# Performance work log

Measured on AMD Instinct MI355X. Metric: run time of the kernel, lower is better.

Reference implementation:

```python
import jax, jax.numpy as jnp
import numpy as np

N = 150000   # total supergraph nodes (entities+events+chains)
D = 128      # embed_size
H = 4        # attention heads
DH = D // H  # head dim
E = 300000   # edges per layer
L = 4        # layer_specs length
A = 8        # edge attr dim
T = 10       # num_edge_type
TIME_SCALE = 24.0
SLOPE = 0.2  # negative_slope


def setup_inputs() -> dict:
    key = jax.random.key(0)
    ks = jax.random.split(key, 16)
    nrm = lambda k, s, sc=1.0: jax.random.normal(k, s, dtype=jnp.float32) * sc
    return {
        'x': nrm(ks[0], (N, D), 0.1),
        'Wq': nrm(ks[1], (L, D, D), D ** -0.5),
        'Wk': nrm(ks[2], (L, D, D), D ** -0.5),
        'Wv': nrm(ks[3], (L, D, D), D ** -0.5),
        'Wskip': nrm(ks[4], (L, D, D), D ** -0.5),
        'Wa': nrm(ks[5], (L, A, D), 0.1),
        'time_w': nrm(ks[6], (D,)),
        'time_b': nrm(ks[7], (D,), 0.1),
        'dist_w': nrm(ks[8], (D,)),
        'dist_b': nrm(ks[9], (D,), 0.1),
        'type_table': nrm(ks[10], (T, D), 0.1),
        'bn_gamma': jnp.ones((L, D), jnp.float32),
        'bn_beta': jnp.zeros((L, D), jnp.float32),
        'beta': jnp.full((L,), 0.5, jnp.float32),
        'edge_attr': jax.random.uniform(ks[11], (L, E, A), dtype=jnp.float32),
        'edge_dt': jax.random.uniform(ks[12], (L, E), dtype=jnp.float32) * TIME_SCALE,
        'edge_ds': jax.random.uniform(ks[13], (L, E), dtype=jnp.float32) * 10.0,
        'edge_index': jax.random.randint(ks[14], (L, 2, E), 0, N),
        'edge_type': jax.random.randint(ks[15], (L, E), 0, T),
    }


def _layer(x, Wq, Wk, Wv, Wskip, Wa, time_w, time_b, dist_w, dist_b,
           type_table, gamma, bvec, beta, attr, dt, ds, ei, et):
    n = x.shape[0]
    src, dst = ei[0], ei[1]
    # continuous time / distance encoders: cos basis (TimeEncoder / 'time' DistanceEncoder)
    te = jnp.cos((dt / TIME_SCALE)[:, None] * time_w + time_b)   # [E,D]
    de = jnp.cos(ds[:, None] * dist_w + dist_b)                  # [E,D]
    # 'add' edge/time fusion: attr MLP + time + dist + edge-type embeddings
    edge_feat = attr @ Wa + te + de + type_table[et]             # [E,D]
    kv_in = x[src] + edge_feat                                   # gather + fuse
    q = (x @ Wq).reshape(n, H, DH)[dst]                          # [E,H,DH]
    k = (kv_in @ Wk).reshape(-1, H, DH)
    v = (kv_in @ Wv).reshape(-1, H, DH)
    logits = (q * k).sum(-1) * (DH ** -0.5)                      # [E,H]
    logits = jnp.where(logits >= 0, logits, SLOPE * logits)      # leaky_relu(negative_slope)
    # segment softmax over incoming edges of each destination node
    m = jax.ops.segment_max(logits, dst, num_segments=n)
    a = jnp.exp(logits - m[dst])
    denom = jax.ops.segment_sum(a, dst, num_segments=n)
    a = a / denom[dst]
    agg = jax.ops.segment_sum(a[..., None] * v, dst, num_segments=n).reshape(n, D)
    # beta-weighted residual (learn_beta) with skip projection
    out = beta * (x @ Wskip) + (1.0 - beta) * agg
    # BatchNorm1d (training-mode batch stats) + ReLU
    mu = out.mean(0)
    var = out.var(0)
    out = (out - mu) * jax.lax.rsqrt(var + 1e-5) * gamma + bvec
    return jax.nn.relu(out)


def reference(x, Wq, Wk, Wv, Wskip, Wa, time_w, time_b, dist_w, dist_b,
              type_table, bn_gamma, bn_beta, beta, edge_attr, edge_dt,
              edge_ds, edge_index, edge_type):
    for l in range(L):  # entity2event, event2event, event2chain (time filter), chain2chain
        x = _layer(x, Wq[l], Wk[l], Wv[l], Wskip[l], Wa[l],
                   time_w, time_b, dist_w, dist_b, type_table,
                   bn_gamma[l], bn_beta[l], beta[l],
                   edge_attr[l], edge_dt[l], edge_ds[l],
                   edge_index[l], edge_type[l])
    return x
```

## Files before the change

kernel.cpp:

```cpp
#include <hip/hip_runtime.h>

typedef unsigned int u32;
typedef unsigned short u16;
typedef short bf16x8 __attribute__((ext_vector_type(8)));
typedef float f32x4 __attribute__((ext_vector_type(4)));

#define N_NODES 150000
#define E_EDGES 300000
#define L_CNT   151552

__device__ __forceinline__ float b2f(u16 h){ return __uint_as_float(((u32)h) << 16); }
__device__ __forceinline__ u16 f2bf(float f){
  u32 u = __float_as_uint(f);
  return (u16)((u + 0x7fffu + ((u >> 16) & 1u)) >> 16);
}

__device__ __forceinline__ f32x4 mfma16(bf16x8 a, bf16x8 b, f32x4 c){
  return __builtin_amdgcn_mfma_f32_16x16x32_bf16(a, b, c, 0, 0, 0);
}

__device__ __forceinline__ int opsw(int r, int k){ return (r * 128 + k) ^ ((r & 7) << 3); }
__device__ __forceinline__ int csw(int r, int n){ return (r * 128 + n) ^ (((r >> 2) & 3) << 3); }

__global__ __launch_bounds__(256)
void k_wt(const float* __restrict__ Wq, const float* __restrict__ Wk,
          const float* __restrict__ Wv, const float* __restrict__ Ws,
          u16* __restrict__ Wt)
{
  const int m = blockIdx.x;
  const float* src = (m < 4 ? Wq : m < 8 ? Wk : m < 12 ? Wv : Ws)
                     + (size_t)(m & 3) * 16384;
  u16* dst = Wt + (size_t)m * 16384;
  const int t = threadIdx.x;
  for (int i = 0; i < 16; ++i) {
    int idx = i * 256 + t;
    int n = idx >> 5;
    int k4 = (idx & 31) << 2;
    ushort4 o;
    o.x = f2bf(src[(k4 + 0) * 128 + n]);
    o.y = f2bf(src[(k4 + 1) * 128 + n]);
    o.z = f2bf(src[(k4 + 2) * 128 + n]);
    o.w = f2bf(src[(k4 + 3) * 128 + n]);
    *(ushort4*)(dst + n * 128 + k4) = o;
  }
}


__device__ __forceinline__ void acc_zero(f32x4 (&acc)[2][8])
{
  #pragma unroll
  for (int a = 0; a < 2; ++a)
    #pragma unroll
    for (int b = 0; b < 8; ++b) {
      acc[a][b][0] = 0.f; acc[a][b][1] = 0.f;
      acc[a][b][2] = 0.f; acc[a][b][3] = 0.f;
    }
}

__device__ __forceinline__ void acc_to_lds(u16* Cs, f32x4 (&acc)[2][8], int lane)
{
  const int lr = lane & 15;
  const int g4 = (lane >> 4) << 2;
  #pragma unroll
  for (int mt = 0; mt < 2; ++mt)
    #pragma unroll
    for (int nt = 0; nt < 8; ++nt)
      #pragma unroll
      for (int j = 0; j < 4; ++j)
        Cs[csw(mt * 16 + g4 + j, nt * 16 + lr)] = f2bf(acc[mt][nt][j]);
}

__device__ __forceinline__ void lds_to_global(const u16* Cs, u16* __restrict__ G,
                                              int base, int nr, int lane)
{
  #pragma unroll
  for (int i = 0; i < 8; ++i) {
    int idx = i * 64 + lane;
    int r = idx >> 4, n8 = (idx & 15) << 3;
    if (r < nr) {
      uint4 v = *(const uint4*)(Cs + csw(r, n8));
      *(uint4*)(G + (size_t)(base + r) * 128 + n8) = v;
    }
  }
}


__global__ __launch_bounds__(256)
void k_hist(const int* __restrict__ eidx, int* __restrict__ counts)
{
  const int l = blockIdx.y;
  const int e = blockIdx.x * 256 + threadIdx.x;
  if (e < E_EDGES) {
    int dst = eidx[(size_t)l * 2 * E_EDGES + E_EDGES + e];
    atomicAdd(&counts[(size_t)l * L_CNT + dst], 1);
  }
}

__global__ __launch_bounds__(256)
void k_scan1(const int* __restrict__ counts, int* __restrict__ rowptr,
             int* __restrict__ bsum)
{
  __shared__ int sh[256];
  const int b = blockIdx.x, l = blockIdx.y;
  const int t = threadIdx.x;
  const int* c = counts + (size_t)l * L_CNT + b * 2048;
  int* rp = rowptr + (size_t)l * L_CNT + b * 2048;
  int v[8]; int s = 0;
  #pragma unroll
  for (int j = 0; j < 8; ++j) { v[j] = c[t * 8 + j]; s += v[j]; }
  sh[t] = s; __syncthreads();
  for (int off = 1; off < 256; off <<= 1) {
    int x = (t >= off) ? sh[t - off] : 0;
    __syncthreads();
    sh[t] += x;
    __syncthreads();
  }
  int excl = (t == 0) ? 0 : sh[t - 1];
  if (t == 255) bsum[l * 128 + b] = sh[255];
  int run = excl;
  #pragma unroll
  for (int j = 0; j < 8; ++j) { rp[t * 8 + j] = run; run += v[j]; }
}

__global__ __launch_bounds__(128)
void k_scan2(int* __restrict__ bsum)
{
  __shared__ int sh[128];
  const int l = blockIdx.x, t = threadIdx.x;
  int v = (t < 74) ? bsum[l * 128 + t] : 0;
  sh[t] = v; __syncthreads();
  for (int off = 1; off < 128; off <<= 1) {
    int x = (t >= off) ? sh[t - off] : 0;
    __syncthreads();
    sh[t] += x;
    __syncthreads();
  }
  int excl = (t == 0) ? 0 : sh[t - 1];
  if (t < 74) bsum[l * 128 + t] = excl;
}

__global__ __launch_bounds__(256)
void k_scan3(int* __restrict__ rowptr, int* __restrict__ tmp,
             const int* __restrict__ bsum)
{
  const int l = blockIdx.y;
  const int q = blockIdx.x * 256 + threadIdx.x;
  int v = rowptr[(size_t)l * L_CNT + q] + bsum[l * 128 + (q >> 11)];
  rowptr[(size_t)l * L_CNT + q] = v;
  tmp[(size_t)l * L_CNT + q] = v;
}

__global__ __launch_bounds__(256)
void k_scatter(const int* __restrict__ eidx, int* __restrict__ tmp,
               int* __restrict__ sorted)
{
  const int l = blockIdx.y;
  const int e = blockIdx.x * 256 + threadIdx.x;
  if (e < E_EDGES) {
    int dst = eidx[(size_t)l * 2 * E_EDGES + E_EDGES + e];
    int pos = atomicAdd(&tmp[(size_t)l * L_CNT + dst], 1);
    sorted[(size_t)l * E_EDGES + pos] = e;
  }
}


template<int XF32>
__global__ __launch_bounds__(256)
void gemm_qs(const void* __restrict__ xg, const u16* __restrict__ WtQ,
             const u16* __restrict__ WtS, u16* __restrict__ Qo,
             u16* __restrict__ So)
{
  __shared__ __align__(16) u16 AsAll[4][4160];
  const int t = threadIdx.x;
  const int w = t >> 6, lane = t & 63;
  u16* As = AsAll[w];
  const int lr = lane & 15, hi = lane >> 4;
  const int tile = blockIdx.x * 4 + w;
  const int row0 = tile * 32;
  if (row0 >= N_NODES) return;
  const int nr = min(32, N_NODES - row0);
  const int g = lane >> 5;
  const int c4 = (lane & 31) << 2;

  #pragma unroll
  for (int i = 0; i < 16; ++i) {
    int r = i * 2 + g;
    ushort4 o = make_ushort4(0, 0, 0, 0);
    if (r < nr) {
      if (XF32) {
        float4 v = *(const float4*)((const float*)xg + (size_t)(row0 + r) * 128 + c4);
        o.x = f2bf(v.x); o.y = f2bf(v.y); o.z = f2bf(v.z); o.w = f2bf(v.w);
      } else {
        o = *(const ushort4*)((const u16*)xg + (size_t)(row0 + r) * 128 + c4);
      }
    }
    *(ushort4*)(As + opsw(r, c4)) = o;
  }

  f32x4 qacc[2][8], sacc[2][8];
  acc_zero(qacc); acc_zero(sacc);
  #pragma unroll
  for (int ks = 0; ks < 4; ++ks) {
    const int kb = ks * 32 + hi * 8;
    bf16x8 a0 = *(const bf16x8*)(As + opsw(lr, kb));
    bf16x8 a1 = *(const bf16x8*)(As + opsw(16 + lr, kb));
    #pragma unroll
    for (int nb = 0; nb < 8; ++nb) {
      bf16x8 bq = *(const bf16x8*)(WtQ + (nb * 16 + lr) * 128 + kb);
      bf16x8 bs = *(const bf16x8*)(WtS + (nb * 16 + lr) * 128 + kb);
      qacc[0][nb] = mfma16(a0, bq, qacc[0][nb]);
      qacc[1][nb] = mfma16(a1, bq, qacc[1][nb]);
      sacc[0][nb] = mfma16(a0, bs, sacc[0][nb]);
      sacc[1][nb] = mfma16(a1, bs, sacc[1][nb]);
    }
  }
  acc_to_lds(As, qacc, lane);
  lds_to_global(As, Qo, row0, nr, lane);
  acc_to_lds(As, sacc, lane);
  lds_to_global(As, So, row0, nr, lane);
}


template<int XF32>
__global__ __launch_bounds__(256)
void edge_pass(const void* __restrict__ xg, const u16* __restrict__ WtK,
               const u16* __restrict__ WtV, const float* __restrict__ Wa,
               const float* __restrict__ tw, const float* __restrict__ tb,
               const float* __restrict__ dw, const float* __restrict__ db,
               const float* __restrict__ ttab, const float* __restrict__ attr,
               const float* __restrict__ dt, const float* __restrict__ dsv,
               const int* __restrict__ srcA, const int* __restrict__ dstA,
               const int* __restrict__ etA, const int* __restrict__ sortedE,
               const u16* __restrict__ Qb, float* __restrict__ logits,
               u16* __restrict__ Vs)
{
  __shared__ __align__(16) u16 AsAll[4][4160];
  __shared__ int dstShAll[4][32];
  const int t = threadIdx.x;
  const int w = t >> 6, lane = t & 63;
  u16* As = AsAll[w];
  int* dstSh = dstShAll[w];
  const int lr = lane & 15, hi = lane >> 4;
  const int tile = blockIdx.x * 4 + w;
  const int e0 = tile * 32;
  if (e0 >= E_EDGES) return;
  const int ne = min(32, E_EDGES - e0);
  const int g = lane >> 5;
  const int c4 = (lane & 31) << 2;

  float4 tw4 = *(const float4*)(tw + c4);
  float4 tb4 = *(const float4*)(tb + c4);
  float4 dw4 = *(const float4*)(dw + c4);
  float4 db4 = *(const float4*)(db + c4);
  float4 wa4[8];
  #pragma unroll
  for (int a = 0; a < 8; ++a) wa4[a] = *(const float4*)(Wa + a * 128 + c4);

  #pragma unroll
  for (int i = 0; i < 16; ++i) {
    int r = i * 2 + g;
    ushort4 o = make_ushort4(0, 0, 0, 0);
    if (r < ne) {
      int eid = sortedE[e0 + r];
      if ((lane & 31) == 0) dstSh[r] = dstA[eid];
      int et = etA[eid];
      float dtn = dt[eid] * (1.0f / 24.0f);
      float dss = dsv[eid];
      float4 tt4 = *(const float4*)(ttab + et * 128 + c4);
      float f0 = __cosf(fmaf(dtn, tw4.x, tb4.x)) + __cosf(fmaf(dss, dw4.x, db4.x)) + tt4.x;
      float f1 = __cosf(fmaf(dtn, tw4.y, tb4.y)) + __cosf(fmaf(dss, dw4.y, db4.y)) + tt4.y;
      float f2 = __cosf(fmaf(dtn, tw4.z, tb4.z)) + __cosf(fmaf(dss, dw4.z, db4.z)) + tt4.z;
      float f3 = __cosf(fmaf(dtn, tw4.w, tb4.w)) + __cosf(fmaf(dss, dw4.w, db4.w)) + tt4.w;
      const float* ap = attr + (size_t)eid * 8;
      #pragma unroll
      for (int a = 0; a < 8; ++a) {
        float aa = ap[a];
        f0 = fmaf(aa, wa4[a].x, f0);
        f1 = fmaf(aa, wa4[a].y, f1);
        f2 = fmaf(aa, wa4[a].z, f2);
        f3 = fmaf(aa, wa4[a].w, f3);
      }
      int src = srcA[eid];
      float x0, x1, x2, x3;
      if (XF32) {
        float4 xr = *(const float4*)((const float*)xg + (size_t)src * 128 + c4);
        x0 = xr.x; x1 = xr.y; x2 = xr.z; x3 = xr.w;
      } else {
        ushort4 xr = *(const ushort4*)((const u16*)xg + (size_t)src * 128 + c4);
        x0 = b2f(xr.x); x1 = b2f(xr.y); x2 = b2f(xr.z); x3 = b2f(xr.w);
      }
      o.x = f2bf(x0 + f0);
      o.y = f2bf(x1 + f1);
      o.z = f2bf(x2 + f2);
      o.w = f2bf(x3 + f3);
    } else {
      if ((lane & 31) == 0) dstSh[r] = 0;
    }
    *(ushort4*)(As + opsw(r, c4)) = o;
  }

  f32x4 kacc[2][8];
  acc_zero(kacc);
  #pragma unroll
  for (int ks = 0; ks < 4; ++ks) {
    const int kb = ks * 32 + hi * 8;
    bf16x8 ef0 = *(const bf16x8*)(As + opsw(lr, kb));
    bf16x8 ef1 = *(const bf16x8*)(As + opsw(16 + lr, kb));
    #pragma unroll
    for (int nb = 0; nb < 8; ++nb) {
      bf16x8 af = *(const bf16x8*)(WtK + (nb * 16 + lr) * 128 + kb);
      kacc[0][nb] = mfma16(af, ef0, kacc[0][nb]);
      kacc[1][nb] = mfma16(af, ef1, kacc[1][nb]);
    }
  }

  #pragma unroll
  for (int eb = 0; eb < 2; ++eb) {
    int el = eb * 16 + lr;
    int dstn = dstSh[el];
    float hs[4] = {0.f, 0.f, 0.f, 0.f};
    #pragma unroll
    for (int nb = 0; nb < 8; ++nb) {
      ushort4 q = *(const ushort4*)(Qb + (size_t)dstn * 128 + nb * 16 + hi * 4);
      hs[nb >> 1] += b2f(q.x) * kacc[eb][nb][0] + b2f(q.y) * kacc[eb][nb][1]
                   + b2f(q.z) * kacc[eb][nb][2] + b2f(q.w) * kacc[eb][nb][3];
    }
    #pragma unroll
    for (int h = 0; h < 4; ++h) {
      hs[h] += __shfl_xor(hs[h], 16, 64);
      hs[h] += __shfl_xor(hs[h], 32, 64);
      hs[h] *= 0.17677669529663687f;
      hs[h] = (hs[h] >= 0.f) ? hs[h] : 0.2f * hs[h];
    }
    if (lane < 16 && el < ne)
      *(float4*)(logits + (size_t)(e0 + el) * 4) = make_float4(hs[0], hs[1], hs[2], hs[3]);
  }

  f32x4 vacc[2][8];
  acc_zero(vacc);
  #pragma unroll
  for (int ks = 0; ks < 4; ++ks) {
    const int kb = ks * 32 + hi * 8;
    bf16x8 af0 = *(const bf16x8*)(As + opsw(lr, kb));
    bf16x8 af1 = *(const bf16x8*)(As + opsw(16 + lr, kb));
    #pragma unroll
    for (int nb = 0; nb < 8; ++nb) {
      bf16x8 bf = *(const bf16x8*)(WtV + (nb * 16 + lr) * 128 + kb);
      vacc[0][nb] = mfma16(af0, bf, vacc[0][nb]);
      vacc[1][nb] = mfma16(af1, bf, vacc[1][nb]);
    }
  }
  acc_to_lds(As, vacc, lane);
  lds_to_global(As, Vs, e0, ne, lane);
}

__global__ __launch_bounds__(256)
void node_agg(const u16* __restrict__ Vs, const float* __restrict__ logits,
              const int* __restrict__ rowptr, const u16* __restrict__ S,
              const float* __restrict__ betaP, float* __restrict__ pre,
              float* __restrict__ colsum, float* __restrict__ colsumsq)
{
  __shared__ float red[1024];
  const int t = threadIdx.x;
  const int g = t >> 5;
  const int lane = t & 31;
  const int d0 = lane * 4;
  const int h = lane >> 3;
  const float beta = *betaP;
  const float omb = 1.f - beta;
  float s4[4] = {0.f, 0.f, 0.f, 0.f};
  float q4[4] = {0.f, 0.f, 0.f, 0.f};
  for (int rep = 0; rep < 16; ++rep) {
    int n = blockIdx.x * 128 + rep * 8 + g;
    if (n < N_NODES) {
      int rs = rowptr[n], re = rowptr[n + 1];
      float m = -1e30f;
      for (int i = rs; i < re; ++i)
        m = fmaxf(m, logits[(size_t)i * 4 + h]);
      float den = 0.f;
      float a0 = 0.f, a1 = 0.f, a2 = 0.f, a3 = 0.f;
      for (int i = rs; i < re; ++i) {
        float wgt = __expf(logits[(size_t)i * 4 + h] - m);
        den += wgt;
        ushort4 v = *(const ushort4*)(Vs + (size_t)i * 128 + d0);
        a0 = fmaf(wgt, b2f(v.x), a0);
        a1 = fmaf(wgt, b2f(v.y), a1);
        a2 = fmaf(wgt, b2f(v.z), a2);
        a3 = fmaf(wgt, b2f(v.w), a3);
      }
      float inv = (den > 0.f) ? (omb / den) : 0.f;
      ushort4 sv = *(const ushort4*)(S + (size_t)n * 128 + d0);
      float p0 = fmaf(beta, b2f(sv.x), a0 * inv);
      float p1 = fmaf(beta, b2f(sv.y), a1 * inv);
      float p2 = fmaf(beta, b2f(sv.z), a2 * inv);
      float p3 = fmaf(beta, b2f(sv.w), a3 * inv);
      *(float4*)(pre + (size_t)n * 128 + d0) = make_float4(p0, p1, p2, p3);
      s4[0] += p0; s4[1] += p1; s4[2] += p2; s4[3] += p3;
      q4[0] += p0 * p0; q4[1] += p1 * p1; q4[2] += p2 * p2; q4[3] += p3 * p3;
    }
  }
  *(float4*)(&red[g * 128 + d0]) = make_float4(s4[0], s4[1], s4[2], s4[3]);
  __syncthreads();
  if (t < 128) {
    float tot = 0.f;
    #pragma unroll
    for (int gg = 0; gg < 8; ++gg) tot += red[gg * 128 + t];
    atomicAdd(&colsum[t], tot);
  }
  __syncthreads();
  *(float4*)(&red[g * 128 + d0]) = make_float4(q4[0], q4[1], q4[2], q4[3]);
  __syncthreads();
  if (t < 128) {
    float tot = 0.f;
    #pragma unroll
    for (int gg = 0; gg < 8; ++gg) tot += red[gg * 128 + t];
    atomicAdd(&colsumsq[t], tot);
  }
}

template<int LAST>
__global__ __launch_bounds__(256)
void bn_apply(const float* __restrict__ pre, const float* __restrict__ colsum,
              const float* __restrict__ colsumsq, const float* __restrict__ gamma,
              const float* __restrict__ bvec, u16* __restrict__ outbf,
              float* __restrict__ outf)
{
  const int idx = blockIdx.x * 256 + threadIdx.x;
  const int n = idx >> 5;
  const int d0 = (idx & 31) * 4;
  const float invN = 1.f / 150000.f;
  float4 p = *(const float4*)(pre + (size_t)n * 128 + d0);
  float4 cs = *(const float4*)(colsum + d0);
  float4 cq = *(const float4*)(colsumsq + d0);
  float4 gm = *(const float4*)(gamma + d0);
  float4 bv = *(const float4*)(bvec + d0);
  float mu, var, y;
  mu = cs.x * invN; var = cq.x * invN - mu * mu;
  y = (p.x - mu) * rsqrtf(var + 1e-5f) * gm.x + bv.x; p.x = fmaxf(y, 0.f);
  mu = cs.y * invN; var = cq.y * invN - mu * mu;
  y = (p.y - mu) * rsqrtf(var + 1e-5f) * gm.y + bv.y; p.y = fmaxf(y, 0.f);
  mu = cs.z * invN; var = cq.z * invN - mu * mu;
  y = (p.z - mu) * rsqrtf(var + 1e-5f) * gm.z + bv.z; p.z = fmaxf(y, 0.f);
  mu = cs.w * invN; var = cq.w * invN - mu * mu;
  y = (p.w - mu) * rsqrtf(var + 1e-5f) * gm.w + bv.w; p.w = fmaxf(y, 0.f);
  if (LAST) {
    *(float4*)(outf + (size_t)n * 128 + d0) = p;
  } else {
    ushort4 o;
    o.x = f2bf(p.x); o.y = f2bf(p.y); o.z = f2bf(p.z); o.w = f2bf(p.w);
    *(ushort4*)(outbf + (size_t)n * 128 + d0) = o;
  }
}

extern "C" void kernel_launch(void* const* d_in, const int* in_sizes, int n_in,
                              void* d_out, int out_size, void* d_ws, size_t ws_size,
                              hipStream_t stream)
{
  const float* x0    = (const float*)d_in[0];
  const float* Wq    = (const float*)d_in[1];
  const float* Wk    = (const float*)d_in[2];
  const float* Wv    = (const float*)d_in[3];
  const float* Wsk   = (const float*)d_in[4];
  const float* Wa    = (const float*)d_in[5];
  const float* tw    = (const float*)d_in[6];
  const float* tb    = (const float*)d_in[7];
  const float* dw    = (const float*)d_in[8];
  const float* db    = (const float*)d_in[9];
  const float* ttab  = (const float*)d_in[10];
  const float* gam   = (const float*)d_in[11];
  const float* bet   = (const float*)d_in[12];
  const float* betaP = (const float*)d_in[13];
  const float* attr  = (const float*)d_in[14];
  const float* dt    = (const float*)d_in[15];
  const float* dsv   = (const float*)d_in[16];
  const int*   eidx  = (const int*)d_in[17];
  const int*   etyp  = (const int*)d_in[18];

  char* p = (char*)d_ws;
  u16* xbf  = (u16*)p;       p += 38400000;
  u16* Q    = (u16*)p;       p += 38400000;
  u16* S    = (u16*)p;       p += 38400000;
  u16* Vs   = (u16*)p;       p += 76800000;
  float* logits = (float*)p; p += 4800000;
  int* rowptr = (int*)p;     p += 4 * L_CNT * 4;
  int* tmp    = (int*)p;     p += 4 * L_CNT * 4;
  int* sorted = (int*)p;     p += 4 * E_EDGES * 4;
  int* bsum   = (int*)p;     p += 4 * 128 * 4;
  float* colsum   = (float*)p; p += 512;
  float* colsumsq = (float*)p; p += 512;
  u16* Wt = (u16*)p;         p += 16 * 16384 * 2;

  float* pre = (float*)d_out;

  k_wt<<<16, 256, 0, stream>>>(Wq, Wk, Wv, Wsk, Wt);
  hipMemsetAsync(tmp, 0, 4 * L_CNT * 4, stream);
  k_hist<<<dim3(1172, 4), 256, 0, stream>>>(eidx, tmp);
  k_scan1<<<dim3(74, 4), 256, 0, stream>>>(tmp, rowptr, bsum);
  k_scan2<<<4, 128, 0, stream>>>(bsum);
  k_scan3<<<dim3(592, 4), 256, 0, stream>>>(rowptr, tmp, bsum);
  k_scatter<<<dim3(1172, 4), 256, 0, stream>>>(eidx, tmp, sorted);

  for (int l = 0; l < 4; ++l) {
    const int* srcA = eidx + (size_t)l * 600000;
    const int* dstA = srcA + 300000;
    const int* sortedE = sorted + (size_t)l * E_EDGES;
    const int* rpl = rowptr + (size_t)l * L_CNT;
    const u16* WtQl = Wt + (size_t)l * 16384;
    const u16* WtKl = Wt + (size_t)(4 + l) * 16384;
    const u16* WtVl = Wt + (size_t)(8 + l) * 16384;
    const u16* WtSl = Wt + (size_t)(12 + l) * 16384;
    const float* Wal = Wa + (size_t)l * 1024;
    const float* attrl = attr + (size_t)l * 2400000;
    const float* dtl = dt + (size_t)l * 300000;
    const float* dsl = dsv + (size_t)l * 300000;
    const int* etl = etyp + (size_t)l * 300000;

    hipMemsetAsync(colsum, 0, 1024, stream);

    if (l == 0) {
      gemm_qs<1><<<1172, 256, 0, stream>>>((const void*)x0, WtQl, WtSl, Q, S);
      edge_pass<1><<<2344, 256, 0, stream>>>(
          (const void*)x0, WtKl, WtVl, Wal, tw, tb, dw, db, ttab, attrl,
          dtl, dsl, srcA, dstA, etl, sortedE, Q, logits, Vs);
    } else {
      gemm_qs<0><<<1172, 256, 0, stream>>>((const void*)xbf, WtQl, WtSl, Q, S);
      edge_pass<0><<<2344, 256, 0, stream>>>(
          (const void*)xbf, WtKl, WtVl, Wal, tw, tb, dw, db, ttab, attrl,
          dtl, dsl, srcA, dstA, etl, sortedE, Q, logits, Vs);
    }

    node_agg<<<1172, 256, 0, stream>>>(Vs, logits, rpl, S, betaP + l,
                                       pre, colsum, colsumsq);

    if (l < 3)
      bn_apply<0><<<18750, 256, 0, stream>>>(pre, colsum, colsumsq,
                                             gam + (size_t)l * 128,
                                             bet + (size_t)l * 128, xbf, nullptr);
    else
      bn_apply<1><<<18750, 256, 0, stream>>>(pre, colsum, colsumsq,
                                             gam + (size_t)l * 128,
                                             bet + (size_t)l * 128,
                                             nullptr, (float*)d_out);
  }
}
```

Baseline: 1.707 ms.

## Pack sorted per-edge metadata in scatter, shrink blocks and split Q/skip GEMM

The scatter kernel now runs once per layer and writes a packed 32-byte record per edge into destination-sorted order: src, dst with edge type, scaled dt, ds, and bf16-packed attributes. The edge pass then reads these records contiguously instead of making indirect gathers through a sorted index. The Q and skip GEMMs are split across a second grid dimension, blocks shrink to 128 threads with a min-blocks launch bound, and the K/V accumulators are computed in halves to lower register pressure and raise occupancy. The risks are precision loss from bf16 edge attributes and four extra scatter launches.

```diff
diff --git a/kernel.cpp b/kernel.cpp
--- a/kernel.cpp
+++ b/kernel.cpp
@@ -9,10 +9,15 @@
 #define E_EDGES 300000
 #define L_CNT   151552
 
+__device__ __forceinline__ float blo(u32 u){ return __uint_as_float(u << 16); }
+__device__ __forceinline__ float bhi(u32 u){ return __uint_as_float(u & 0xffff0000u); }
 __device__ __forceinline__ float b2f(u16 h){ return __uint_as_float(((u32)h) << 16); }
 __device__ __forceinline__ u16 f2bf(float f){
   u32 u = __float_as_uint(f);
   return (u16)((u + 0x7fffu + ((u >> 16) & 1u)) >> 16);
+}
+__device__ __forceinline__ u32 pack2(float a, float b){
+  return (u32)f2bf(a) | ((u32)f2bf(b) << 16);
 }
 
 __device__ __forceinline__ f32x4 mfma16(bf16x8 a, bf16x8 b, f32x4 c){
@@ -45,31 +50,6 @@
   }
 }
 
-
-__device__ __forceinline__ void acc_zero(f32x4 (&acc)[2][8])
-{
-  #pragma unroll
-  for (int a = 0; a < 2; ++a)
-    #pragma unroll
-    for (int b = 0; b < 8; ++b) {
-      acc[a][b][0] = 0.f; acc[a][b][1] = 0.f;
-      acc[a][b][2] = 0.f; acc[a][b][3] = 0.f;
-    }
-}
-
-__device__ __forceinline__ void acc_to_lds(u16* Cs, f32x4 (&acc)[2][8], int lane)
-{
-  const int lr = lane & 15;
-  const int g4 = (lane >> 4) << 2;
-  #pragma unroll
-  for (int mt = 0; mt < 2; ++mt)
-    #pragma unroll
-    for (int nt = 0; nt < 8; ++nt)
-      #pragma unroll
-      for (int j = 0; j < 4; ++j)
-        Cs[csw(mt * 16 + g4 + j, nt * 16 + lr)] = f2bf(acc[mt][nt][j]);
-}
-
 __device__ __forceinline__ void lds_to_global(const u16* Cs, u16* __restrict__ G,
                                               int base, int nr, int lane)
 {
@@ -151,31 +131,49 @@
 }
 
 __global__ __launch_bounds__(256)
-void k_scatter(const int* __restrict__ eidx, int* __restrict__ tmp,
-               int* __restrict__ sorted)
-{
-  const int l = blockIdx.y;
+void k_scatter(const int* __restrict__ srcP, const int* __restrict__ dstP,
+               const int* __restrict__ etP, const float* __restrict__ dtP,
+               const float* __restrict__ dsP, const float* __restrict__ attrP,
+               int* __restrict__ tmpL, u32* __restrict__ meta)
+{
   const int e = blockIdx.x * 256 + threadIdx.x;
   if (e < E_EDGES) {
-    int dst = eidx[(size_t)l * 2 * E_EDGES + E_EDGES + e];
-    int pos = atomicAdd(&tmp[(size_t)l * L_CNT + dst], 1);
-    sorted[(size_t)l * E_EDGES + pos] = e;
+    int dst = dstP[e];
+    int pos = atomicAdd(&tmpL[dst], 1);
+    int src = srcP[e];
+    int et  = etP[e];
+    float dtn = dtP[e] * (1.0f / 24.0f);
+    float dsv = dsP[e];
+    float4 aA = *(const float4*)(attrP + (size_t)e * 8);
+    float4 aB = *(const float4*)(attrP + (size_t)e * 8 + 4);
+    uint4 r0, r1;
+    r0.x = (u32)src;
+    r0.y = (u32)dst | ((u32)et << 20);
+    r0.z = __float_as_uint(dtn);
+    r0.w = __float_as_uint(dsv);
+    r1.x = pack2(aA.x, aA.y); r1.y = pack2(aA.z, aA.w);
+    r1.z = pack2(aB.x, aB.y); r1.w = pack2(aB.z, aB.w);
+    u32* mp = meta + (size_t)pos * 8;
+    *(uint4*)mp = r0;
+    *(uint4*)(mp + 4) = r1;
   }
 }
 
 
 template<int XF32>
-__global__ __launch_bounds__(256)
+__global__ __launch_bounds__(128, 5)
 void gemm_qs(const void* __restrict__ xg, const u16* __restrict__ WtQ,
              const u16* __restrict__ WtS, u16* __restrict__ Qo,
              u16* __restrict__ So)
 {
-  __shared__ __align__(16) u16 AsAll[4][4160];
+  __shared__ __align__(16) u16 AsAll[2][4160];
+  const u16* Wt = blockIdx.y ? WtS : WtQ;
+  u16* C = blockIdx.y ? So : Qo;
   const int t = threadIdx.x;
   const int w = t >> 6, lane = t & 63;
   u16* As = AsAll[w];
   const int lr = lane & 15, hi = lane >> 4;
-  const int tile = blockIdx.x * 4 + w;
+  const int tile = blockIdx.x * 2 + w;
   const int row0 = tile * 32;
   if (row0 >= N_NODES) return;
   const int nr = min(32, N_NODES - row0);
@@ -197,8 +195,14 @@
     *(ushort4*)(As + opsw(r, c4)) = o;
   }
 
-  f32x4 qacc[2][8], sacc[2][8];
-  acc_zero(qacc); acc_zero(sacc);
+  f32x4 acc[2][8];
+  #pragma unroll
+  for (int a = 0; a < 2; ++a)
+    #pragma unroll
+    for (int b = 0; b < 8; ++b) {
+      acc[a][b][0] = 0.f; acc[a][b][1] = 0.f;
+      acc[a][b][2] = 0.f; acc[a][b][3] = 0.f;
+    }
   #pragma unroll
   for (int ks = 0; ks < 4; ++ks) {
     const int kb = ks * 32 + hi * 8;
@@ -206,42 +210,41 @@
     bf16x8 a1 = *(const bf16x8*)(As + opsw(16 + lr, kb));
     #pragma unroll
     for (int nb = 0; nb < 8; ++nb) {
-      bf16x8 bq = *(const bf16x8*)(WtQ + (nb * 16 + lr) * 128 + kb);
-      bf16x8 bs = *(const bf16x8*)(WtS + (nb * 16 + lr) * 128 + kb);
-      qacc[0][nb] = mfma16(a0, bq, qacc[0][nb]);
-      qacc[1][nb] = mfma16(a1, bq, qacc[1][nb]);
-      sacc[0][nb] = mfma16(a0, bs, sacc[0][nb]);
-      sacc[1][nb] = mfma16(a1, bs, sacc[1][nb]);
-    }
-  }
-  acc_to_lds(As, qacc, lane);
-  lds_to_global(As, Qo, row0, nr, lane);
-  acc_to_lds(As, sacc, lane);
-  lds_to_global(As, So, row0, nr, lane);
+      bf16x8 b = *(const bf16x8*)(Wt + (nb * 16 + lr) * 128 + kb);
+      acc[0][nb] = mfma16(a0, b, acc[0][nb]);
+      acc[1][nb] = mfma16(a1, b, acc[1][nb]);
+    }
+  }
+  const int g4 = hi << 2;
+  #pragma unroll
+  for (int mt = 0; mt < 2; ++mt)
+    #pragma unroll
+    for (int nt = 0; nt < 8; ++nt)
+      #pragma unroll
+      for (int j = 0; j < 4; ++j)
+        As[csw(mt * 16 + g4 + j, nt * 16 + lr)] = f2bf(acc[mt][nt][j]);
+  lds_to_global(As, C, row0, nr, lane);
 }
 
 
 template<int XF32>
-__global__ __launch_bounds__(256)
+__global__ __launch_bounds__(128, 5)
 void edge_pass(const void* __restrict__ xg, const u16* __restrict__ WtK,
                const u16* __restrict__ WtV, const float* __restrict__ Wa,
                const float* __restrict__ tw, const float* __restrict__ tb,
                const float* __restrict__ dw, const float* __restrict__ db,
-               const float* __restrict__ ttab, const float* __restrict__ attr,
-               const float* __restrict__ dt, const float* __restrict__ dsv,
-               const int* __restrict__ srcA, const int* __restrict__ dstA,
-               const int* __restrict__ etA, const int* __restrict__ sortedE,
+               const float* __restrict__ ttab, const u32* __restrict__ meta,
                const u16* __restrict__ Qb, float* __restrict__ logits,
                u16* __restrict__ Vs)
 {
-  __shared__ __align__(16) u16 AsAll[4][4160];
-  __shared__ int dstShAll[4][32];
+  __shared__ __align__(16) u16 AsAll[2][4160];
+  __shared__ int dstShAll[2][32];
   const int t = threadIdx.x;
   const int w = t >> 6, lane = t & 63;
   u16* As = AsAll[w];
   int* dstSh = dstShAll[w];
   const int lr = lane & 15, hi = lane >> 4;
-  const int tile = blockIdx.x * 4 + w;
+  const int tile = blockIdx.x * 2 + w;
   const int e0 = tile * 32;
   if (e0 >= E_EDGES) return;
   const int ne = min(32, E_EDGES - e0);
@@ -261,26 +264,28 @@
     int r = i * 2 + g;
     ushort4 o = make_ushort4(0, 0, 0, 0);
     if (r < ne) {
-      int eid = sortedE[e0 + r];
-      if ((lane & 31) == 0) dstSh[r] = dstA[eid];
-      int et = etA[eid];
-      float dtn = dt[eid] * (1.0f / 24.0f);
-      float dss = dsv[eid];
+      const u32* mp = meta + (size_t)(e0 + r) * 8;
+      uint4 m0 = *(const uint4*)mp;
+      uint4 m1 = *(const uint4*)(mp + 4);
+      int src = (int)m0.x;
+      if ((lane & 31) == 0) dstSh[r] = (int)(m0.y & 0xFFFFFu);
+      int et = (int)(m0.y >> 20);
+      float dtn = __uint_as_float(m0.z);
+      float dss = __uint_as_float(m0.w);
       float4 tt4 = *(const float4*)(ttab + et * 128 + c4);
       float f0 = __cosf(fmaf(dtn, tw4.x, tb4.x)) + __cosf(fmaf(dss, dw4.x, db4.x)) + tt4.x;
       float f1 = __cosf(fmaf(dtn, tw4.y, tb4.y)) + __cosf(fmaf(dss, dw4.y, db4.y)) + tt4.y;
       float f2 = __cosf(fmaf(dtn, tw4.z, tb4.z)) + __cosf(fmaf(dss, dw4.z, db4.z)) + tt4.z;
       float f3 = __cosf(fmaf(dtn, tw4.w, tb4.w)) + __cosf(fmaf(dss, dw4.w, db4.w)) + tt4.w;
-      const float* ap = attr + (size_t)eid * 8;
+      float aa[8] = { blo(m1.x), bhi(m1.x), blo(m1.y), bhi(m1.y),
+                      blo(m1.z), bhi(m1.z), blo(m1.w), bhi(m1.w) };
       #pragma unroll
       for (int a = 0; a < 8; ++a) {
-        float aa = ap[a];
-        f0 = fmaf(aa, wa4[a].x, f0);
-        f1 = fmaf(aa, wa4[a].y, f1);
-        f2 = fmaf(aa, wa4[a].z, f2);
-        f3 = fmaf(aa, wa4[a].w, f3);
+        f0 = fmaf(aa[a], wa4[a].x, f0);
+        f1 = fmaf(aa[a], wa4[a].y, f1);
+        f2 = fmaf(aa[a], wa4[a].z, f2);
+        f3 = fmaf(aa[a], wa4[a].w, f3);
       }
-      int src = srcA[eid];
       float x0, x1, x2, x3;
       if (XF32) {
         float4 xr = *(const float4*)((const float*)xg + (size_t)src * 128 + c4);
@@ -299,31 +304,31 @@
     *(ushort4*)(As + opsw(r, c4)) = o;
   }
 
-  f32x4 kacc[2][8];
-  acc_zero(kacc);
-  #pragma unroll
-  for (int ks = 0; ks < 4; ++ks) {
-    const int kb = ks * 32 + hi * 8;
-    bf16x8 ef0 = *(const bf16x8*)(As + opsw(lr, kb));
-    bf16x8 ef1 = *(const bf16x8*)(As + opsw(16 + lr, kb));
-    #pragma unroll
-    for (int nb = 0; nb < 8; ++nb) {
-      bf16x8 af = *(const bf16x8*)(WtK + (nb * 16 + lr) * 128 + kb);
-      kacc[0][nb] = mfma16(af, ef0, kacc[0][nb]);
-      kacc[1][nb] = mfma16(af, ef1, kacc[1][nb]);
-    }
-  }
-
   #pragma unroll
   for (int eb = 0; eb < 2; ++eb) {
+    f32x4 kacc[8];
+    #pragma unroll
+    for (int b = 0; b < 8; ++b) {
+      kacc[b][0] = 0.f; kacc[b][1] = 0.f; kacc[b][2] = 0.f; kacc[b][3] = 0.f;
+    }
+    #pragma unroll
+    for (int ks = 0; ks < 4; ++ks) {
+      const int kb = ks * 32 + hi * 8;
+      bf16x8 ef = *(const bf16x8*)(As + opsw(eb * 16 + lr, kb));
+      #pragma unroll
+      for (int nb = 0; nb < 8; ++nb) {
+        bf16x8 af = *(const bf16x8*)(WtK + (nb * 16 + lr) * 128 + kb);
+        kacc[nb] = mfma16(af, ef, kacc[nb]);
+      }
+    }
     int el = eb * 16 + lr;
     int dstn = dstSh[el];
     float hs[4] = {0.f, 0.f, 0.f, 0.f};
     #pragma unroll
     for (int nb = 0; nb < 8; ++nb) {
       ushort4 q = *(const ushort4*)(Qb + (size_t)dstn * 128 + nb * 16 + hi * 4);
-      hs[nb >> 1] += b2f(q.x) * kacc[eb][nb][0] + b2f(q.y) * kacc[eb][nb][1]
-                   + b2f(q.z) * kacc[eb][nb][2] + b2f(q.w) * kacc[eb][nb][3];
+      hs[nb >> 1] += b2f(q.x) * kacc[nb][0] + b2f(q.y) * kacc[nb][1]
+                   + b2f(q.z) * kacc[nb][2] + b2f(q.w) * kacc[nb][3];
     }
     #pragma unroll
     for (int h = 0; h < 4; ++h) {
@@ -336,21 +341,30 @@
       *(float4*)(logits + (size_t)(e0 + el) * 4) = make_float4(hs[0], hs[1], hs[2], hs[3]);
   }
 
-  f32x4 vacc[2][8];
-  acc_zero(vacc);
-  #pragma unroll
-  for (int ks = 0; ks < 4; ++ks) {
-    const int kb = ks * 32 + hi * 8;
-    bf16x8 af0 = *(const bf16x8*)(As + opsw(lr, kb));
-    bf16x8 af1 = *(const bf16x8*)(As + opsw(16 + lr, kb));
-    #pragma unroll
-    for (int nb = 0; nb < 8; ++nb) {
-      bf16x8 bf = *(const bf16x8*)(WtV + (nb * 16 + lr) * 128 + kb);
-      vacc[0][nb] = mfma16(af0, bf, vacc[0][nb]);
-      vacc[1][nb] = mfma16(af1, bf, vacc[1][nb]);
-    }
-  }
-  acc_to_lds(As, vacc, lane);
+  const int g4 = hi << 2;
+  #pragma unroll
+  for (int mt = 0; mt < 2; ++mt) {
+    f32x4 vacc[8];
+    #pragma unroll
+    for (int b = 0; b < 8; ++b) {
+      vacc[b][0] = 0.f; vacc[b][1] = 0.f; vacc[b][2] = 0.f; vacc[b][3] = 0.f;
+    }
+    #pragma unroll
+    for (int ks = 0; ks < 4; ++ks) {
+      const int kb = ks * 32 + hi * 8;
+      bf16x8 af = *(const bf16x8*)(As + opsw(mt * 16 + lr, kb));
+      #pragma unroll
+      for (int nb = 0; nb < 8; ++nb) {
+        bf16x8 bf = *(const bf16x8*)(WtV + (nb * 16 + lr) * 128 + kb);
+        vacc[nb] = mfma16(af, bf, vacc[nb]);
+      }
+    }
+    #pragma unroll
+    for (int nt = 0; nt < 8; ++nt)
+      #pragma unroll
+      for (int j = 0; j < 4; ++j)
+        As[csw(mt * 16 + g4 + j, nt * 16 + lr)] = f2bf(vacc[nt][j]);
+  }
   lds_to_global(As, Vs, e0, ne, lane);
 }
 
@@ -484,11 +498,11 @@
   float* logits = (float*)p; p += 4800000;
   int* rowptr = (int*)p;     p += 4 * L_CNT * 4;
   int* tmp    = (int*)p;     p += 4 * L_CNT * 4;
-  int* sorted = (int*)p;     p += 4 * E_EDGES * 4;
   int* bsum   = (int*)p;     p += 4 * 128 * 4;
   float* colsum   = (float*)p; p += 512;
   float* colsumsq = (float*)p; p += 512;
   u16* Wt = (u16*)p;         p += 16 * 16384 * 2;
+  u32* meta = (u32*)p;       p += (size_t)E_EDGES * 32;
 
   float* pre = (float*)d_out;
 
@@ -498,35 +512,32 @@
   k_scan1<<<dim3(74, 4), 256, 0, stream>>>(tmp, rowptr, bsum);
   k_scan2<<<4, 128, 0, stream>>>(bsum);
   k_scan3<<<dim3(592, 4), 256, 0, stream>>>(rowptr, tmp, bsum);
-  k_scatter<<<dim3(1172, 4), 256, 0, stream>>>(eidx, tmp, sorted);
 
   for (int l = 0; l < 4; ++l) {
     const int* srcA = eidx + (size_t)l * 600000;
     const int* dstA = srcA + 300000;
-    const int* sortedE = sorted + (size_t)l * E_EDGES;
     const int* rpl = rowptr + (size_t)l * L_CNT;
     const u16* WtQl = Wt + (size_t)l * 16384;
     const u16* WtKl = Wt + (size_t)(4 + l) * 16384;
     const u16* WtVl = Wt + (size_t)(8 + l) * 16384;
     const u16* WtSl = Wt + (size_t)(12 + l) * 16384;
     const float* Wal = Wa + (size_t)l * 1024;
-    const float* attrl = attr + (size_t)l * 2400000;
-    const float* dtl = dt + (size_t)l * 300000;
-    const float* dsl = dsv + (size_t)l * 300000;
-    const int* etl = etyp + (size_t)l * 300000;
+
+    k_scatter<<<1172, 256, 0, stream>>>(
+        srcA, dstA, etyp + (size_t)l * 300000, dt + (size_t)l * 300000,
+        dsv + (size_t)l * 300000, attr + (size_t)l * 2400000,
+        tmp + (size_t)l * L_CNT, meta);
 
     hipMemsetAsync(colsum, 0, 1024, stream);
 
     if (l == 0) {
-      gemm_qs<1><<<1172, 256, 0, stream>>>((const void*)x0, WtQl, WtSl, Q, S);
-      edge_pass<1><<<2344, 256, 0, stream>>>(
-          (const void*)x0, WtKl, WtVl, Wal, tw, tb, dw, db, ttab, attrl,
-          dtl, dsl, srcA, dstA, etl, sortedE, Q, logits, Vs);
+      gemm_qs<1><<<dim3(2344, 2), 128, 0, stream>>>((const void*)x0, WtQl, WtSl, Q, S);
+      edge_pass<1><<<4688, 128, 0, stream>>>(
+          (const void*)x0, WtKl, WtVl, Wal, tw, tb, dw, db, ttab, meta, Q, logits, Vs);
     } else {
-      gemm_qs<0><<<1172, 256, 0, stream>>>((const void*)xbf, WtQl, WtSl, Q, S);
-      edge_pass<0><<<2344, 256, 0, stream>>>(
-          (const void*)xbf, WtKl, WtVl, Wal, tw, tb, dw, db, ttab, attrl,
-          dtl, dsl, srcA, dstA, etl, sortedE, Q, logits, Vs);
+      gemm_qs<0><<<dim3(2344, 2), 128, 0, stream>>>((const void*)xbf, WtQl, WtSl, Q, S);
+      edge_pass<0><<<4688, 128, 0, stream>>>(
+          (const void*)xbf, WtKl, WtVl, Wal, tw, tb, dw, db, ttab, meta, Q, logits, Vs);
     }
 
     node_agg<<<1172, 256, 0, stream>>>(Vs, logits, rpl, S, betaP + l,
```

Result: slower. 2.155 ms (+26.2%).
